# Optimization experiments

Measured on AMD Instinct MI355X. Metric: run time of the kernel, lower is better.

Reference implementation:

```python
import jax, jax.numpy as jnp
import numpy as np

SELF_DIM = 64
OBST_DIM = 32
NUM_LANDMARKS = 8
HID = 128
IN_DIM = SELF_DIM + OBST_DIM  # 96


def setup_inputs() -> dict:
    key = jax.random.key(0)
    ks = jax.random.split(key, 16)
    B = 1024
    obs = jax.random.normal(ks[0], (B, 1, SELF_DIM + 40 + NUM_LANDMARKS * OBST_DIM), dtype=jnp.float32)

    def w(k, shape, fan_in):
        return (jax.random.normal(k, shape, dtype=jnp.float32) / np.sqrt(fan_in)).astype(jnp.float32)

    return {
        "obs": obs,
        "all_neighbor_obs_size": 40,
        "batch_size": B,
        # Hypernet2: Linear(96->128), tanh, Linear(128->96*128), tanh
        "hw1": w(ks[1], (IN_DIM, HID), IN_DIM), "hb1": jnp.zeros((HID,), jnp.float32),
        "hw2": w(ks[2], (HID, IN_DIM * HID), HID), "hb2": jnp.zeros((IN_DIM * HID,), jnp.float32),
        # neighbor_value_mlp: two Linear(128->128) with tanh
        "vw1": w(ks[3], (HID, HID), HID), "vb1": jnp.zeros((HID,), jnp.float32),
        "vw2": w(ks[4], (HID, HID), HID), "vb2": jnp.zeros((HID,), jnp.float32),
        # attention_mlp: Linear(256->128) tanh, Linear(128->128) tanh, Linear(128->1)
        "aw1": w(ks[5], (2 * HID, HID), 2 * HID), "ab1": jnp.zeros((HID,), jnp.float32),
        "aw2": w(ks[6], (HID, HID), HID), "ab2": jnp.zeros((HID,), jnp.float32),
        "aw3": w(ks[7], (HID, 1), HID), "ab3": jnp.zeros((1,), jnp.float32),
    }


def reference(obs, all_neighbor_obs_size, batch_size,
              hw1, hb1, hw2, hb2, vw1, vb1, vw2, vb2,
              aw1, ab1, aw2, ab2, aw3, ab3):
    B = batch_size
    A = obs.shape[1]  # agents per row (1)
    L = NUM_LANDMARKS

    # slice obstacle block and flatten to per-obstacle rows  [B*A*L, OBST_DIM]
    obs_obstacles = obs[:, :, SELF_DIM + all_neighbor_obs_size:].reshape(-1, OBST_DIM)
    # repeat self-obs along dim 1 (torch .repeat(1, L, 1)) -> [B*A*L, SELF_DIM]
    self_rep = jnp.tile(obs[:, :, :SELF_DIM], (1, L, 1)).reshape(-1, SELF_DIM)
    mlp_input = jnp.concatenate([self_rep, obs_obstacles], axis=1)  # [N, 96]
    N = mlp_input.shape[0]

    # Hypernet2 -> per-instance weight [N, 96, HID]
    h = jnp.tanh(mlp_input @ hw1 + hb1)
    w_flat = jnp.tanh(h @ hw2 + hb2)
    obstacle_w = w_flat.reshape(N, IN_DIM, HID)

    # per-instance matvec + tanh  [N, HID]
    emb = jnp.tanh(jnp.einsum('ni,nio->no', mlp_input, obstacle_w))

    # neighbor value MLP
    vals = jnp.tanh(jnp.tanh(emb @ vw1 + vb1) @ vw2 + vb2)

    # mean pooling over landmarks per batch
    emb_mean = emb.reshape(B, -1, HID).mean(axis=1)  # [B, HID]
    # torch mean.repeat(L, 1): tile whole batch block L times (faithful ordering)
    mean_rep = jnp.tile(emb_mean, (L, 1))  # [B*L, HID]

    att_in = jnp.concatenate([emb, mean_rep], axis=1)  # [N, 2*HID]
    a = jnp.tanh(att_in @ aw1 + ab1)
    a = jnp.tanh(a @ aw2 + ab2)
    logits = (a @ aw3 + ab3).reshape(B, -1)  # [B, L]
    att = jax.nn.softmax(logits, axis=1).reshape(-1, 1)  # [N, 1]

    final = (att * vals).reshape(B, -1, HID).sum(axis=1)  # [B, HID]
    return final.reshape(-1, A, HID)
```

## Files before the change

### kernel.cpp

```cpp
#include <hip/hip_runtime.h>

typedef _Float16 f16x8 __attribute__((ext_vector_type(8)));
typedef float f32x4 __attribute__((ext_vector_type(4)));
typedef const __attribute__((address_space(1))) void* as1_cvp;
typedef __attribute__((address_space(3))) void* as3_vp;

__device__ __forceinline__ float tanh_fast(float x){
  float e = __builtin_amdgcn_exp2f(x * 2.88539008177793f);
  return 1.f - 2.f * __builtin_amdgcn_rcpf(1.f + e);
}
__device__ __forceinline__ unsigned short f2h(float f){
  return __builtin_bit_cast(unsigned short, (_Float16)f);
}
__device__ __forceinline__ float h2f(unsigned short u){
  return (float)__builtin_bit_cast(_Float16, u);
}
__device__ __forceinline__ f32x4 mfma16(f16x8 a, f16x8 b, f32x4 c){
  return __builtin_amdgcn_mfma_f32_16x16x32_f16(a, b, c, 0, 0, 0);
}

__device__ __forceinline__ f16x8 ldsA(const unsigned short* buf, int rb, int s, int lane){
  return *(const f16x8*)(buf + (rb*16 + (lane&15))*128 + s*32 + ((lane>>4)<<3));
}

__global__ __launch_bounds__(256) void prep_kernel(
    const float* __restrict__ obs, const float* __restrict__ hw1,
    const float* __restrict__ hb1, const float* __restrict__ hw2,
    const float* __restrict__ vw1, const float* __restrict__ vw2,
    const float* __restrict__ aw1, const float* __restrict__ aw2,
    unsigned short* __restrict__ wt2, unsigned short* __restrict__ vw1t,
    unsigned short* __restrict__ vw2t, unsigned short* __restrict__ aw1t,
    unsigned short* __restrict__ aw2t, unsigned short* __restrict__ h16,
    float* __restrict__ xT){
  int b = blockIdx.x, t = threadIdx.x;
  if (b < 1616){
    __shared__ float tile[32][33];
    const float* in; unsigned short* out; int R, C, bx, by; bool swz;
    if (b < 1536)      { in=hw2; out=wt2;  R=128; C=12288; bx=b%384;      by=b/384; swz=true; }
    else if (b < 1552) { int q=b-1536; in=vw1; out=vw1t; R=128; C=128; bx=q&3; by=q>>2; swz=false; }
    else if (b < 1568) { int q=b-1552; in=vw2; out=vw2t; R=128; C=128; bx=q&3; by=q>>2; swz=false; }
    else if (b < 1600) { int q=b-1568; in=aw1; out=aw1t; R=256; C=128; bx=q&3; by=q>>2; swz=false; }
    else               { int q=b-1600; in=aw2; out=aw2t; R=128; C=128; bx=q&3; by=q>>2; swz=false; }
    int c0=bx*32, r0=by*32, tx=t&31, ty=t>>5;
    #pragma unroll
    for (int j=ty; j<32; j+=8) tile[j][tx] = in[(size_t)(r0+j)*C + c0 + tx];
    __syncthreads();
    if (swz){
      #pragma unroll
      for (int j=ty; j<32; j+=8){
        int col = c0+j, k = r0+tx;
        int i = col>>7, colL = col&127;
        int chalf = colL>>6, c64 = colL&63;
        out[(size_t)(i*2 + chalf)*8192 + c64*128 + (k ^ ((col&15)<<3))] = f2h(tile[tx][j]);
      }
    } else {
      #pragma unroll
      for (int j=ty; j<32; j+=8) out[(size_t)(c0+j)*R + r0 + tx] = f2h(tile[tx][j]);
    }
  } else {
    __shared__ float w_s[96*128];
    __shared__ float x_s[32*97];
    __shared__ float b_s[128];
    int n0 = (b-1616)*32;
    for (int idx=t; idx<96*128; idx+=256) w_s[idx] = hw1[idx];
    if (t < 128) b_s[t] = hb1[t];
    for (int idx=t; idx<32*96; idx+=256){
      int r = idx/96, i = idx - r*96;
      int n = n0 + r; int bb = n>>3, l = n&7;
      x_s[r*97+i] = (i<64) ? obs[bb*360 + i] : obs[bb*360 + 104 + (l<<5) + (i-64)];
    }
    __syncthreads();
    for (int e=t; e<96*32; e+=256){
      int i = e>>5, r = e&31;
      xT[(size_t)i*8192 + n0 + r] = x_s[r*97 + i];
    }
    for (int e=t; e<32*128; e+=256){
      int r = e>>7, o = e&127;
      float acc = b_s[o];
      const float* xr = &x_s[r*97];
      #pragma unroll 4
      for (int i=0;i<96;++i) acc = fmaf(xr[i], w_s[i*128+o], acc);
      h16[(size_t)(n0+r)*128 + o] = f2h(tanh_fast(acc));
    }
  }
}

__device__ __forceinline__ void stage_tile(const unsigned short* gsrc,
                                           unsigned short* lbuf, int t){
  const unsigned short* g = gsrc + t*8;
  unsigned short* l = lbuf + t*8;
  #pragma unroll
  for (int p=0;p<4;++p)
    __builtin_amdgcn_global_load_lds((as1_cvp)(g + p*2048), (as3_vp)(l + p*2048), 16, 0, 0);
}

__global__ __launch_bounds__(256, 4) void k2_hyper(
    const float* __restrict__ xT, const unsigned short* __restrict__ h16,
    const unsigned short* __restrict__ wt2, const float* __restrict__ hb2,
    float* __restrict__ accg){
  __shared__ unsigned short bts[2][8192];
  int t = threadIdx.x, lane = t & 63, rg = t >> 6;
  int bid = blockIdx.x;
  int rt = bid >> 4, chalf = (bid >> 3) & 1, iseg = bid & 7;
  int R0 = rt*128, C0 = chalf*64, ibase = iseg*12;
  int cl   = lane & 15;
  int kof  = (lane>>4) << 3;
  int rloc = (lane>>4) << 2;
  int sx   = cl << 3;

  f16x8 af[2][4];
  #pragma unroll
  for (int rb=0; rb<2; ++rb)
    #pragma unroll
    for (int s=0; s<4; ++s)
      af[rb][s] = *(const f16x8*)(h16 + (size_t)(R0 + rg*32 + rb*16 + cl)*128 + s*32 + kof);

  stage_tile(wt2 + (size_t)(ibase*2 + chalf)*8192, bts[0], t);
  __syncthreads();

  float facc[2][4][4];
  #pragma unroll
  for (int rb=0;rb<2;++rb)
    #pragma unroll
    for (int ch=0;ch<4;++ch)
      #pragma unroll
      for (int reg=0;reg<4;++reg) facc[rb][ch][reg] = 0.f;

  for (int it=0; it<12; ++it){
    const unsigned short* lb = bts[it&1];
    if (it < 11) stage_tile(wt2 + (size_t)((ibase+it+1)*2 + chalf)*8192, bts[(it+1)&1], t);
    f32x4 xa = *(const f32x4*)(xT + (size_t)(ibase+it)*8192 + R0 + rg*32 + rloc);
    f32x4 xb = *(const f32x4*)(xT + (size_t)(ibase+it)*8192 + R0 + rg*32 + 16 + rloc);
    const float* bias_p = hb2 + (ibase+it)*128 + C0;
    #pragma unroll
    for (int ch=0; ch<4; ++ch){
      int c64 = ch*16 + cl;
      const unsigned short* bp = lb + c64*128;
      f16x8 b0 = *(const f16x8*)(bp + ((  0+kof)^sx));
      f16x8 b1 = *(const f16x8*)(bp + (( 32+kof)^sx));
      f16x8 b2 = *(const f16x8*)(bp + (( 64+kof)^sx));
      f16x8 b3 = *(const f16x8*)(bp + (( 96+kof)^sx));
      float bi = bias_p[c64];
      f32x4 a0 = {bi,bi,bi,bi}, a1 = {bi,bi,bi,bi};
      a0 = mfma16(af[0][0], b0, a0); a1 = mfma16(af[1][0], b0, a1);
      a0 = mfma16(af[0][1], b1, a0); a1 = mfma16(af[1][1], b1, a1);
      a0 = mfma16(af[0][2], b2, a0); a1 = mfma16(af[1][2], b2, a1);
      a0 = mfma16(af[0][3], b3, a0); a1 = mfma16(af[1][3], b3, a1);
      #pragma unroll
      for (int reg=0;reg<4;++reg){
        facc[0][ch][reg] = fmaf(xa[reg], tanh_fast(a0[reg]), facc[0][ch][reg]);
        facc[1][ch][reg] = fmaf(xb[reg], tanh_fast(a1[reg]), facc[1][ch][reg]);
      }
    }
    __syncthreads();
  }

  #pragma unroll
  for (int rb=0; rb<2; ++rb)
    #pragma unroll
    for (int ch=0; ch<4; ++ch)
      #pragma unroll
      for (int reg=0; reg<4; ++reg)
        atomicAdd(&accg[(size_t)(R0 + rg*32 + rb*16 + rloc + reg)*128 + C0 + ch*16 + cl],
                  facc[rb][ch][reg]);
}

__global__ __launch_bounds__(256) void k3_mean(const float* __restrict__ accg,
    unsigned short* __restrict__ mean16){
  int t = threadIdx.x, B0 = blockIdx.x*4;
  for (int task=t; task<512; task+=256){
    int bl = task>>7, o = task&127;
    float m = 0.f;
    #pragma unroll
    for (int l=0;l<8;++l)
      m += tanh_fast(accg[(size_t)((B0 + bl)*8 + l)*128 + o]);
    mean16[(size_t)(B0 + bl)*128 + o] = f2h(m * 0.125f);
  }
}

template<int KS>
__device__ __forceinline__ void stage(const unsigned short* inA, const unsigned short* inB,
    const unsigned short* wt, const float* bias, unsigned short* outb, int w, int lane){
  #pragma unroll
  for (int obl=0; obl<2; ++obl){
    int col = ((w*2+obl)<<4) + (lane&15);
    f32x4 a0 = {0.f,0.f,0.f,0.f}, a1v = {0.f,0.f,0.f,0.f};
    #pragma unroll
    for (int s=0;s<KS;++s){
      f16x8 bfr = *(const f16x8*)(wt + (size_t)col*(KS*32) + s*32 + ((lane>>4)<<3));
      f16x8 aa0, aa1;
      if (KS==8 && s>=4){ aa0 = ldsA(inB,0,s-4,lane); aa1 = ldsA(inB,1,s-4,lane); }
      else              { aa0 = ldsA(inA,0,s,lane);   aa1 = ldsA(inA,1,s,lane);   }
      a0  = mfma16(aa0, bfr, a0);
      a1v = mfma16(aa1, bfr, a1v);
    }
    float bb = bias[col];
    #pragma unroll
    for (int reg=0;reg<4;++reg){
      int r0 = ((lane>>4)<<2) + reg;
      outb[r0*128 + col]      = f2h(tanh_fast(a0[reg] + bb));
      outb[(16+r0)*128 + col] = f2h(tanh_fast(a1v[reg] + bb));
    }
  }
}

__global__ __launch_bounds__(256) void k4_mlp(
    const float* __restrict__ accg, const unsigned short* __restrict__ mean16,
    const unsigned short* __restrict__ vw1t, const unsigned short* __restrict__ vw2t,
    const unsigned short* __restrict__ aw1t, const unsigned short* __restrict__ aw2t,
    const float* __restrict__ vb1, const float* __restrict__ vb2,
    const float* __restrict__ ab1, const float* __restrict__ ab2,
    const float* __restrict__ aw3, const float* __restrict__ ab3,
    float* __restrict__ outp){
  __shared__ unsigned short bufE[32*128];
  __shared__ unsigned short bufM[32*128];
  __shared__ unsigned short bufA[32*128];
  __shared__ float fin[4*128];
  __shared__ float lp[32*8];
  __shared__ float att_s[32];
  int t = threadIdx.x, lane = t&63, w = t>>6;
  int R0 = blockIdx.x*32;

  for (int idx=t; idx<4096; idx+=256)
    bufE[idx] = f2h(tanh_fast(accg[(size_t)R0*128 + idx]));
  for (int idx=t; idx<512; idx+=256){
    int r = idx>>4, c8 = (idx&15)<<3;
    int n = R0 + r;
    *(uint4*)(bufM + r*128 + c8) = *(const uint4*)(mean16 + (size_t)(n & 1023)*128 + c8);
  }
  for (int idx=t; idx<512; idx+=256) fin[idx] = 0.f;
  __syncthreads();

  stage<8>(bufE, bufM, aw1t, ab1, bufA, w, lane);
  __syncthreads();
  stage<4>(bufA, nullptr, aw2t, ab2, bufM, w, lane);
  __syncthreads();
  {
    int r = t>>3, seg = t&7;
    float p = 0.f;
    const unsigned short* row = bufM + r*128 + seg*16;
    const float* w3 = aw3 + seg*16;
    #pragma unroll
    for (int k=0;k<16;++k) p += h2f(row[k]) * w3[k];
    lp[r*8+seg] = p;
  }
  __syncthreads();
  if (t < 4){
    float lg[8]; float mx = -1e30f;
    for (int l=0;l<8;++l){
      float s = ab3[0];
      #pragma unroll
      for (int sg=0;sg<8;++sg) s += lp[(t*8+l)*8+sg];
      lg[l] = s; mx = fmaxf(mx, s);
    }
    float sum = 0.f;
    for (int l=0;l<8;++l){ lg[l] = __builtin_amdgcn_exp2f((lg[l]-mx)*1.44269504089f); sum += lg[l]; }
    float inv = __builtin_amdgcn_rcpf(sum);
    for (int l=0;l<8;++l) att_s[t*8+l] = lg[l]*inv;
  }
  __syncthreads();
  stage<4>(bufE, nullptr, vw1t, vb1, bufA, w, lane);
  __syncthreads();
  {
    #pragma unroll
    for (int obl=0; obl<2; ++obl){
      int col = ((w*2+obl)<<4) + (lane&15);
      f32x4 a0 = {0.f,0.f,0.f,0.f}, a1v = {0.f,0.f,0.f,0.f};
      #pragma unroll
      for (int s=0;s<4;++s){
        f16x8 bfr = *(const f16x8*)(vw2t + (size_t)col*128 + s*32 + ((lane>>4)<<3));
        a0  = mfma16(ldsA(bufA,0,s,lane), bfr, a0);
        a1v = mfma16(ldsA(bufA,1,s,lane), bfr, a1v);
      }
      float bb = vb2[col];
      #pragma unroll
      for (int reg=0;reg<4;++reg){
        int r0 = ((lane>>4)<<2) + reg;
        float v0 = tanh_fast(a0[reg]+bb);
        float v1 = tanh_fast(a1v[reg]+bb);
        atomicAdd(&fin[((r0)>>3)*128 + col],    att_s[r0]    * v0);
        atomicAdd(&fin[((16+r0)>>3)*128 + col], att_s[16+r0] * v1);
      }
    }
  }
  __syncthreads();
  for (int idx=t; idx<512; idx+=256){
    int b_loc = idx>>7, o = idx&127;
    outp[(size_t)(R0/8 + b_loc)*128 + o] = fin[idx];
  }
}

extern "C" void kernel_launch(void* const* d_in, const int* in_sizes, int n_in,
                              void* d_out, int out_size, void* d_ws, size_t ws_size,
                              hipStream_t stream){
  const float* obs = (const float*)d_in[0];
  const float* hw1 = (const float*)d_in[3];
  const float* hb1 = (const float*)d_in[4];
  const float* hw2 = (const float*)d_in[5];
  const float* hb2 = (const float*)d_in[6];
  const float* vw1 = (const float*)d_in[7];
  const float* vb1 = (const float*)d_in[8];
  const float* vw2 = (const float*)d_in[9];
  const float* vb2 = (const float*)d_in[10];
  const float* aw1 = (const float*)d_in[11];
  const float* ab1 = (const float*)d_in[12];
  const float* aw2 = (const float*)d_in[13];
  const float* ab2 = (const float*)d_in[14];
  const float* aw3 = (const float*)d_in[15];
  const float* ab3 = (const float*)d_in[16];

  char* ws = (char*)d_ws;
  unsigned short* wt2    = (unsigned short*)(ws);
  unsigned short* mean16 = (unsigned short*)(ws);
  unsigned short* h16    = (unsigned short*)(ws + 3145728);
  float*          accg   = (float*)        (ws + 5242880);
  float*          xT     = (float*)        (ws + 9437184);
  unsigned short* vw1t   = (unsigned short*)(ws + 12582912);
  unsigned short* vw2t   = (unsigned short*)(ws + 12615680);
  unsigned short* aw1t   = (unsigned short*)(ws + 12648448);
  unsigned short* aw2t   = (unsigned short*)(ws + 12713984);
  float* outp = (float*)d_out;

  hipMemsetAsync(accg, 0, 8192*128*sizeof(float), stream);
  prep_kernel<<<1872, 256, 0, stream>>>(obs, hw1, hb1, hw2, vw1, vw2, aw1, aw2,
                                        wt2, vw1t, vw2t, aw1t, aw2t, h16, xT);
  k2_hyper<<<1024, 256, 0, stream>>>(xT, h16, wt2, hb2, accg);
  k3_mean<<<256, 256, 0, stream>>>(accg, mean16);
  k4_mlp<<<256, 256, 0, stream>>>(accg, mean16, vw1t, vw2t, aw1t, aw2t,
                                  vb1, vb2, ab1, ab2, aw3, ab3, outp);
}
```

Before: 124.5 us.

## Re-layout hyper weight tiles, stage x and bias in LDS, fold bias into tanh

The hw2 transpose now writes an unswizzled k-group-major fp16 layout with 16-byte vector stores from fewer prep blocks. The hyper kernel reads B fragments linearly from that layout. It preloads the per-block x and bias slices into shared memory and folds the bias into the exp2 argument instead of seeding the MFMA accumulator. The loop now uses a single explicit vmcnt wait plus barrier at the top instead of two __syncthreads, and the launch bounds become waves_per_eu(3,4). The intent is to cut transpose cost, scattered global loads and sync overhead, at the risk of LDS bank conflicts from the unswizzled reads and more LDS use per block.

```diff
diff --git a/kernel.cpp b/kernel.cpp
--- a/kernel.cpp
+++ b/kernel.cpp
@@ -5,8 +5,10 @@
 typedef const __attribute__((address_space(1))) void* as1_cvp;
 typedef __attribute__((address_space(3))) void* as3_vp;
 
+#define LOG2E2 2.88539008177793f
+
 __device__ __forceinline__ float tanh_fast(float x){
-  float e = __builtin_amdgcn_exp2f(x * 2.88539008177793f);
+  float e = __builtin_amdgcn_exp2f(x * LOG2E2);
   return 1.f - 2.f * __builtin_amdgcn_rcpf(1.f + e);
 }
 __device__ __forceinline__ unsigned short f2h(float f){
@@ -18,7 +20,6 @@
 __device__ __forceinline__ f32x4 mfma16(f16x8 a, f16x8 b, f32x4 c){
   return __builtin_amdgcn_mfma_f32_16x16x32_f16(a, b, c, 0, 0, 0);
 }
-
 __device__ __forceinline__ f16x8 ldsA(const unsigned short* buf, int rb, int s, int lane){
   return *(const f16x8*)(buf + (rb*16 + (lane&15))*128 + s*32 + ((lane>>4)<<3));
 }
@@ -33,35 +34,39 @@
     unsigned short* __restrict__ aw2t, unsigned short* __restrict__ h16,
     float* __restrict__ xT){
   int b = blockIdx.x, t = threadIdx.x;
-  if (b < 1616){
+  if (b < 768){
+    __shared__ float xp[64][33];
+    int i = b >> 3, chalf = (b&7) >> 2, kq = b & 3;
+    int c0 = i*128 + chalf*64, r0 = kq*32;
+    int tx = t & 63, j0 = t >> 6;
+    #pragma unroll
+    for (int j = j0; j < 32; j += 4)
+      xp[tx][j] = hw2[(size_t)(r0+j)*12288 + c0 + tx];
+    __syncthreads();
+    int c = t & 63, kgl = t >> 6;
+    unsigned short us[8];
+    #pragma unroll
+    for (int q=0;q<8;++q) us[q] = f2h(xp[c][kgl*8 + q]);
+    size_t dst = (size_t)(i*2 + chalf)*8192 + (size_t)(kq*4 + kgl)*512 + c*8;
+    *(uint4*)(wt2 + dst) = *(uint4*)us;
+  } else if (b < 848){
     __shared__ float tile[32][33];
-    const float* in; unsigned short* out; int R, C, bx, by; bool swz;
-    if (b < 1536)      { in=hw2; out=wt2;  R=128; C=12288; bx=b%384;      by=b/384; swz=true; }
-    else if (b < 1552) { int q=b-1536; in=vw1; out=vw1t; R=128; C=128; bx=q&3; by=q>>2; swz=false; }
-    else if (b < 1568) { int q=b-1552; in=vw2; out=vw2t; R=128; C=128; bx=q&3; by=q>>2; swz=false; }
-    else if (b < 1600) { int q=b-1568; in=aw1; out=aw1t; R=256; C=128; bx=q&3; by=q>>2; swz=false; }
-    else               { int q=b-1600; in=aw2; out=aw2t; R=128; C=128; bx=q&3; by=q>>2; swz=false; }
+    const float* in; unsigned short* out; int R, bx, by;
+    if (b < 784)      { int q=b-768; in=vw1; out=vw1t; R=128; bx=q&3; by=q>>2; }
+    else if (b < 800) { int q=b-784; in=vw2; out=vw2t; R=128; bx=q&3; by=q>>2; }
+    else if (b < 832) { int q=b-800; in=aw1; out=aw1t; R=256; bx=q&3; by=q>>2; }
+    else              { int q=b-832; in=aw2; out=aw2t; R=128; bx=q&3; by=q>>2; }
     int c0=bx*32, r0=by*32, tx=t&31, ty=t>>5;
     #pragma unroll
-    for (int j=ty; j<32; j+=8) tile[j][tx] = in[(size_t)(r0+j)*C + c0 + tx];
+    for (int j=ty; j<32; j+=8) tile[j][tx] = in[(size_t)(r0+j)*128 + c0 + tx];
     __syncthreads();
-    if (swz){
-      #pragma unroll
-      for (int j=ty; j<32; j+=8){
-        int col = c0+j, k = r0+tx;
-        int i = col>>7, colL = col&127;
-        int chalf = colL>>6, c64 = colL&63;
-        out[(size_t)(i*2 + chalf)*8192 + c64*128 + (k ^ ((col&15)<<3))] = f2h(tile[tx][j]);
-      }
-    } else {
-      #pragma unroll
-      for (int j=ty; j<32; j+=8) out[(size_t)(c0+j)*R + r0 + tx] = f2h(tile[tx][j]);
-    }
+    #pragma unroll
+    for (int j=ty; j<32; j+=8) out[(size_t)(c0+j)*R + r0 + tx] = f2h(tile[tx][j]);
   } else {
     __shared__ float w_s[96*128];
     __shared__ float x_s[32*97];
     __shared__ float b_s[128];
-    int n0 = (b-1616)*32;
+    int n0 = (b-848)*32;
     for (int idx=t; idx<96*128; idx+=256) w_s[idx] = hw1[idx];
     if (t < 128) b_s[t] = hb1[t];
     for (int idx=t; idx<32*96; idx+=256){
@@ -94,19 +99,30 @@
     __builtin_amdgcn_global_load_lds((as1_cvp)(g + p*2048), (as3_vp)(l + p*2048), 16, 0, 0);
 }
 
-__global__ __launch_bounds__(256, 4) void k2_hyper(
-    const float* __restrict__ xT, const unsigned short* __restrict__ h16,
-    const unsigned short* __restrict__ wt2, const float* __restrict__ hb2,
-    float* __restrict__ accg){
+__global__ __launch_bounds__(256) __attribute__((amdgpu_waves_per_eu(3,4)))
+void k2_hyper(const float* __restrict__ xT, const unsigned short* __restrict__ h16,
+              const unsigned short* __restrict__ wt2, const float* __restrict__ hb2,
+              float* __restrict__ accg){
   __shared__ unsigned short bts[2][8192];
+  __shared__ float x_s[12*128];
+  __shared__ float bias_s[12*64];
   int t = threadIdx.x, lane = t & 63, rg = t >> 6;
   int bid = blockIdx.x;
   int rt = bid >> 4, chalf = (bid >> 3) & 1, iseg = bid & 7;
   int R0 = rt*128, C0 = chalf*64, ibase = iseg*12;
   int cl   = lane & 15;
-  int kof  = (lane>>4) << 3;
-  int rloc = (lane>>4) << 2;
-  int sx   = cl << 3;
+  int g    = lane >> 4;
+  int kof  = g << 3;
+  int rloc = g << 2;
+
+  for (int idx=t; idx<12*128; idx+=256){
+    int il = idx>>7, r = idx&127;
+    x_s[idx] = xT[(size_t)(ibase+il)*8192 + R0 + r];
+  }
+  for (int idx=t; idx<12*64; idx+=256){
+    int il = idx>>6, c = idx&63;
+    bias_s[idx] = hb2[(ibase+il)*128 + C0 + c];
+  }
 
   f16x8 af[2][4];
   #pragma unroll
@@ -116,7 +132,6 @@
       af[rb][s] = *(const f16x8*)(h16 + (size_t)(R0 + rg*32 + rb*16 + cl)*128 + s*32 + kof);
 
   stage_tile(wt2 + (size_t)(ibase*2 + chalf)*8192, bts[0], t);
-  __syncthreads();
 
   float facc[2][4][4];
   #pragma unroll
@@ -126,33 +141,41 @@
       #pragma unroll
       for (int reg=0;reg<4;++reg) facc[rb][ch][reg] = 0.f;
 
+  const f32x4 zero4 = {0.f,0.f,0.f,0.f};
+
   for (int it=0; it<12; ++it){
+    asm volatile("s_waitcnt vmcnt(0)" ::: "memory");
+    __builtin_amdgcn_s_barrier();
+    __builtin_amdgcn_sched_barrier(0);
     const unsigned short* lb = bts[it&1];
     if (it < 11) stage_tile(wt2 + (size_t)((ibase+it+1)*2 + chalf)*8192, bts[(it+1)&1], t);
-    f32x4 xa = *(const f32x4*)(xT + (size_t)(ibase+it)*8192 + R0 + rg*32 + rloc);
-    f32x4 xb = *(const f32x4*)(xT + (size_t)(ibase+it)*8192 + R0 + rg*32 + 16 + rloc);
-    const float* bias_p = hb2 + (ibase+it)*128 + C0;
+
+    f32x4 xa = *(const f32x4*)(x_s + it*128 + rg*32 + rloc);
+    f32x4 xb = *(const f32x4*)(x_s + it*128 + rg*32 + 16 + rloc);
     #pragma unroll
     for (int ch=0; ch<4; ++ch){
       int c64 = ch*16 + cl;
-      const unsigned short* bp = lb + c64*128;
-      f16x8 b0 = *(const f16x8*)(bp + ((  0+kof)^sx));
-      f16x8 b1 = *(const f16x8*)(bp + (( 32+kof)^sx));
-      f16x8 b2 = *(const f16x8*)(bp + (( 64+kof)^sx));
-      f16x8 b3 = *(const f16x8*)(bp + (( 96+kof)^sx));
-      float bi = bias_p[c64];
-      f32x4 a0 = {bi,bi,bi,bi}, a1 = {bi,bi,bi,bi};
+      const unsigned short* bp = lb + c64*8 + g*512;
+      f16x8 b0 = *(const f16x8*)(bp);
+      f16x8 b1 = *(const f16x8*)(bp + 2048);
+      f16x8 b2 = *(const f16x8*)(bp + 4096);
+      f16x8 b3 = *(const f16x8*)(bp + 6144);
+      float bi2 = bias_s[it*64 + c64] * LOG2E2;
+      f32x4 a0 = zero4, a1 = zero4;
       a0 = mfma16(af[0][0], b0, a0); a1 = mfma16(af[1][0], b0, a1);
       a0 = mfma16(af[0][1], b1, a0); a1 = mfma16(af[1][1], b1, a1);
       a0 = mfma16(af[0][2], b2, a0); a1 = mfma16(af[1][2], b2, a1);
       a0 = mfma16(af[0][3], b3, a0); a1 = mfma16(af[1][3], b3, a1);
       #pragma unroll
       for (int reg=0;reg<4;++reg){
-        facc[0][ch][reg] = fmaf(xa[reg], tanh_fast(a0[reg]), facc[0][ch][reg]);
-        facc[1][ch][reg] = fmaf(xb[reg], tanh_fast(a1[reg]), facc[1][ch][reg]);
+        float e0 = __builtin_amdgcn_exp2f(fmaf(a0[reg], LOG2E2, bi2));
+        float e1 = __builtin_amdgcn_exp2f(fmaf(a1[reg], LOG2E2, bi2));
+        float t0 = 1.f - 2.f*__builtin_amdgcn_rcpf(1.f + e0);
+        float t1 = 1.f - 2.f*__builtin_amdgcn_rcpf(1.f + e1);
+        facc[0][ch][reg] = fmaf(xa[reg], t0, facc[0][ch][reg]);
+        facc[1][ch][reg] = fmaf(xb[reg], t1, facc[1][ch][reg]);
       }
     }
-    __syncthreads();
   }
 
   #pragma unroll
@@ -322,7 +345,7 @@
   float* outp = (float*)d_out;
 
   hipMemsetAsync(accg, 0, 8192*128*sizeof(float), stream);
-  prep_kernel<<<1872, 256, 0, stream>>>(obs, hw1, hb1, hw2, vw1, vw2, aw1, aw2,
+  prep_kernel<<<1104, 256, 0, stream>>>(obs, hw1, hb1, hw2, vw1, vw2, aw1, aw2,
                                         wt2, vw1t, vw2t, aw1t, aw2t, h16, xT);
   k2_hyper<<<1024, 256, 0, stream>>>(xT, h16, wt2, hb2, accg);
   k3_mean<<<256, 256, 0, stream>>>(accg, mean16);
```

Result: faster. 118.6 us (-4.7%).
